# Kernel tuning notes

Measured on AMD Instinct MI355X. Metric: run time of the kernel, lower is better.

## Reference

```python
import jax, jax.numpy as jnp
import numpy as np

PI = float(np.pi)
TWO_PI = 2.0 * PI
LOG_2PI = float(np.log(TWO_PI))
N_FFT = 1024
LOG_N = 10
N_MAX = min(N_FFT, 2000)  # evaluate_z term cap


def _bitrev_indices(N, num_bits):
    idx = np.arange(N)
    rev = np.zeros(N, dtype=np.int32)
    v = idx.copy()
    for _ in range(num_bits):
        rev = (rev << 1) | (v & 1)
        v >>= 1
    return rev

_BITREV = jnp.asarray(_bitrev_indices(N_FFT, LOG_N))


def fft_fused(x_re, x_im):
    """Radix-2 DIT FFT with bit-reversal load, mirroring the Triton kernel.
    x_re/x_im: [B, N]. Returns (y_re, y_im)."""
    B, N = x_re.shape
    y = (x_re + 1j * x_im).astype(jnp.complex64)[:, _BITREV]
    for stage in range(LOG_N):
        s = 1 << stage          # half butterfly size (stride)
        # twiddles W_k = exp(-2*pi*i*k/(2s)), k in [0, s)
        k = jnp.arange(s)
        w = jnp.exp((-TWO_PI * 1j / (2 * s)) * k).astype(jnp.complex64)
        yg = y.reshape(B, N // (2 * s), 2, s)
        upper = yg[:, :, 0, :]
        lower = yg[:, :, 1, :] * w  # broadcast over [B, groups, s]
        y = jnp.concatenate([upper + lower, upper - lower], axis=-1).reshape(B, N)
    return jnp.real(y), jnp.imag(y)


def evaluate_z(t):
    """Riemann-Siegel Z(t) cosine sum with dynamic term count, masked."""
    t_half = t * 0.5
    theta = t_half * (jnp.log(t) - LOG_2PI) - t_half - PI / 8.0
    theta = theta + 1.0 / (48.0 * t)
    n = jnp.arange(1, N_MAX + 1, dtype=t.dtype)
    log_n = jnp.log(n)
    rsqrt_n = jax.lax.rsqrt(n)
    # [P, N_MAX] outer product of phases
    phases = t[:, None] * log_n[None, :] - theta[:, None]
    terms = rsqrt_n[None, :] * jnp.cos(phases)
    n_terms = jnp.clip(jnp.sqrt(jax.lax.stop_gradient(t) / TWO_PI).astype(jnp.int32), 10, N_MAX)
    mask = jnp.arange(N_MAX)[None, :] < n_terms[:, None]
    return 2.0 * jnp.sum(jnp.where(mask, terms, 0.0), axis=-1)


def setup_inputs() -> dict:
    key = jax.random.key(0)
    k1, k2, k3 = jax.random.split(key, 3)
    x_re = jax.random.normal(k1, (16384, N_FFT), dtype=jnp.float32)
    x_im = jax.random.normal(k2, (16384, N_FFT), dtype=jnp.float32)
    # evaluation points t in [1000, 101000)
    t = 1000.0 + 100000.0 * jax.random.uniform(k3, (262144,), dtype=jnp.float32)
    return {"x_re": x_re, "x_im": x_im, "t": t}


def reference(x_re, x_im, t):
    y_re, y_im = fft_fused(x_re, x_im)
    Z = evaluate_z(t)
    return (y_re, y_im, Z)
```

## Files before the change

### kernel.cpp

```cpp
#include <hip/hip_runtime.h>
#include <math.h>

#define INV_2PI_D 0.15915494309189535

#define LDSYNC() asm volatile("s_waitcnt lgkmcnt(0)" ::: "memory")

__device__ __forceinline__ void bfly(float& ar, float& ai, float& br, float& bi,
                                     float wr, float wi) {
    const float tr = wr * br - wi * bi;
    const float ti = wr * bi + wi * br;
    br = ar - tr; bi = ai - ti;
    ar = ar + tr; ai = ai + ti;
}

__device__ __forceinline__ void wrev(float rev, float& c, float& s) {
    s = __builtin_amdgcn_sinf(rev);
    c = __builtin_amdgcn_cosf(rev);
}

__device__ __forceinline__ void fft_row(
    const float* __restrict__ xre, const float* __restrict__ xim,
    float* __restrict__ yre, float* __restrict__ yim,
    float2* __restrict__ s,
    int row)
{
    const int lane = (int)(threadIdx.x & 63u);
    const size_t base = (size_t)row << 10;

    float re[16], im[16];

    const int rev6l = (int)(__brev((unsigned)lane) >> 26);
    const int REV4[16] = {0,8,4,12,2,10,6,14,1,9,5,13,3,11,7,15};
    const float* xr = xre + base + rev6l;
    const float* xi = xim + base + rev6l;
#pragma unroll
    for (int r = 0; r < 16; ++r) {
        re[r] = xr[REV4[r] << 6];
        im[r] = xi[REV4[r] << 6];
    }

    const int lo = lane & 15;
    const int hl = lane >> 4;
    const float lof = (float)lo;

    float c8a[8], s8a[8];
#pragma unroll
    for (int m = 0; m < 8; ++m)
        wrev(-(16.0f * (float)m + lof) * (1.0f / 256.0f), c8a[m], s8a[m]);
    float c4a[4], s4a[4];
#pragma unroll
    for (int m = 0; m < 4; ++m)
        wrev(-(16.0f * (float)m + lof) * (1.0f / 128.0f), c4a[m], s4a[m]);
    float c2a[2], s2a[2];
#pragma unroll
    for (int m = 0; m < 2; ++m)
        wrev(-(16.0f * (float)m + lof) * (1.0f / 64.0f), c2a[m], s2a[m]);
    float c1a, s1a;
    wrev(-lof * (1.0f / 32.0f), c1a, s1a);

    const float W8R[8] = {1.f, 0.9238795325112867f, 0.7071067811865476f,
                          0.3826834323650898f, 0.f, -0.3826834323650898f,
                          -0.7071067811865476f, -0.9238795325112867f};
    const float W8I[8] = {0.f, -0.3826834323650898f, -0.7071067811865476f,
                          -0.9238795325112867f, -1.f, -0.9238795325112867f,
                          -0.7071067811865476f, -0.3826834323650898f};
#pragma unroll
    for (int st = 0; st < 4; ++st) {
        const int S = 1 << st;
#pragma unroll
        for (int rl = 0; rl < 16; ++rl) {
            if (rl & S) continue;
            const int k8 = (rl & (S - 1)) * (8 >> st);
            bfly(re[rl], im[rl], re[rl | S], im[rl | S], W8R[k8], W8I[k8]);
        }
    }

    {
        float2* w = s + 17 * lane;
#pragma unroll
        for (int r = 0; r < 16; ++r) w[r] = make_float2(re[r], im[r]);
    }
    LDSYNC();
    float2* rw = s + 272 * hl + lo;
#pragma unroll
    for (int r = 0; r < 16; ++r) {
        const float2 v = rw[17 * r];
        re[r] = v.x; im[r] = v.y;
    }
    LDSYNC();

#pragma unroll
    for (int rl = 0; rl < 16; ++rl) if (!(rl & 1))
        bfly(re[rl], im[rl], re[rl|1], im[rl|1], c1a, s1a);
#pragma unroll
    for (int rl = 0; rl < 16; ++rl) if (!(rl & 2))
        bfly(re[rl], im[rl], re[rl|2], im[rl|2], c2a[rl & 1], s2a[rl & 1]);
#pragma unroll
    for (int rl = 0; rl < 16; ++rl) if (!(rl & 4))
        bfly(re[rl], im[rl], re[rl|4], im[rl|4], c4a[rl & 3], s4a[rl & 3]);
#pragma unroll
    for (int rl = 0; rl < 16; ++rl) if (!(rl & 8))
        bfly(re[rl], im[rl], re[rl|8], im[rl|8], c8a[rl & 7], s8a[rl & 7]);

    const float lf = (float)lane;
    float cz8[8], sz8[8];
#pragma unroll
    for (int m = 0; m < 8; ++m)
        wrev(-(64.0f * (float)m + lf) * (1.0f / 1024.0f), cz8[m], sz8[m]);
    float cz4[4], sz4[4];
#pragma unroll
    for (int m = 0; m < 4; ++m)
        wrev(-(64.0f * (float)m + lf) * (1.0f / 512.0f), cz4[m], sz4[m]);

#pragma unroll
    for (int r = 0; r < 16; ++r) rw[17 * r] = make_float2(re[r], im[r]);
    LDSYNC();
    {
        const float2* rb = s + 17 * hl + lo;
#pragma unroll
        for (int r = 0; r < 16; ++r) {
            const float2 v = rb[68 * r];
            re[r] = v.x; im[r] = v.y;
        }
    }
    LDSYNC();

#pragma unroll
    for (int rl = 0; rl < 16; ++rl) if (!(rl & 4))
        bfly(re[rl], im[rl], re[rl|4], im[rl|4], cz4[rl & 3], sz4[rl & 3]);
#pragma unroll
    for (int rl = 0; rl < 16; ++rl) if (!(rl & 8))
        bfly(re[rl], im[rl], re[rl|8], im[rl|8], cz8[rl & 7], sz8[rl & 7]);

    float* yr = yre + base + lane;
    float* yi = yim + base + lane;
#pragma unroll
    for (int r = 0; r < 16; ++r) {
        yr[r << 6] = re[r];
        yi[r << 6] = im[r];
    }
}

__global__ __launch_bounds__(256) void table_kernel(float* __restrict__ ws) {
    const int i = (int)(blockIdx.x * 256 + threadIdx.x);
    if (i < 1024) {
        const double nd = (double)(i + 1);
        ws[i]        = (float)log(nd);
        ws[1024 + i] = (float)(1.0 / sqrt(nd));
    }
}

__device__ void z_eval(const float* __restrict__ tin, float* __restrict__ zout,
                       const float* __restrict__ ws, int zblock, int n,
                       float* __restrict__ buf)
{
    for (int i = (int)threadIdx.x; i < 512; i += 256)
        reinterpret_cast<float4*>(buf)[i] = reinterpret_cast<const float4*>(ws)[i];
    __syncthreads();
    const float* slog = buf;
    const float* srsq = buf + 1024;

    const int gid = zblock * 256 + (int)threadIdx.x;
    if (gid >= n) return;

    const float t  = tin[gid];
    const float th = __fmul_rn(t, 0.5f);
    const float logt = (float)log((double)t);
    float theta = __fsub_rn(__fsub_rn(__fmul_rn(th, __fsub_rn(logt, 1.8378770664093453f)), th),
                            0.39269908169872414f);
    theta = __fadd_rn(theta, __fdiv_rn(1.0f, __fmul_rn(48.0f, t)));

    int nt = (int)sqrtf(__fdiv_rn(t, 6.283185307179586f));
    nt = min(max(nt, 10), 1024);

    float acc = 0.0f;
    for (int i = 0; i < nt; ++i) {
        const float p = __fsub_rn(__fmul_rn(t, slog[i]), theta);
        const double rev = (double)p * INV_2PI_D;
        const double fr  = rev - rint(rev);
        const float  c   = __builtin_amdgcn_cosf((float)fr);
        acc = __fmaf_rn(srsq[i], c, acc);
    }
    zout[gid] = __fmul_rn(2.0f, acc);
}

__global__ __launch_bounds__(256, 4) void fused_kernel(
    const float* __restrict__ xre, const float* __restrict__ xim,
    const float* __restrict__ tin, const float* __restrict__ ws,
    float* __restrict__ yre, float* __restrict__ yim, float* __restrict__ zout,
    int z_blocks, int nrows, int nz)
{
    __shared__ float2 s[4][1088];

    const int b = (int)blockIdx.x;
    if (b < z_blocks) {
        z_eval(tin, zout, ws, b, nz, reinterpret_cast<float*>(&s[0][0]));
    } else {
        const int wid = (int)(threadIdx.x >> 6);
        const int row = ((b - z_blocks) << 2) | wid;
        if (row < nrows)
            fft_row(xre, xim, yre, yim, s[wid], row);
    }
}

extern "C" void kernel_launch(void* const* d_in, const int* in_sizes, int n_in,
                              void* d_out, int out_size, void* d_ws, size_t ws_size,
                              hipStream_t stream)
{
    const float* xre = (const float*)d_in[0];
    const float* xim = (const float*)d_in[1];
    const float* t   = (const float*)d_in[2];

    const size_t nfft = (size_t)in_sizes[0];
    const int nrows = (int)(nfft >> 10);
    const int nz    = in_sizes[2];

    float* yre = (float*)d_out;
    float* yim = yre + nfft;
    float* z   = yre + 2 * nfft;
    float* ws  = (float*)d_ws;

    table_kernel<<<4, 256, 0, stream>>>(ws);

    const int f_blocks = (nrows + 3) >> 2;
    const int z_blocks = (nz + 255) >> 8;
    fused_kernel<<<z_blocks + f_blocks, 256, 0, stream>>>(
        xre, xim, t, ws, yre, yim, z, z_blocks, nrows, nz);
}
```

Baseline: 59.73 us.

## Replace LDS transposes in FFT with cross-lane DPP/swizzle butterfly stages

Restructures the per-row 1024-point FFT so the first six stages run across lanes using DPP moves, ds_swizzle and shfl_xor instead of two LDS transposes. Inputs are loaded as contiguous float4 vectors in a new bit-reversed mapping, and the last four stages stay in registers with per-stage twiddles. This removes the LDS traffic for the FFT and shrinks shared memory to the Z-table buffer only. In exchange each cross-lane stage computes both butterfly outputs per lane (roughly double the FLOPs) and adds many permute instructions.

```diff
diff --git a/kernel.cpp b/kernel.cpp
--- a/kernel.cpp
+++ b/kernel.cpp
@@ -3,7 +3,56 @@
 
 #define INV_2PI_D 0.15915494309189535
 
-#define LDSYNC() asm volatile("s_waitcnt lgkmcnt(0)" ::: "memory")
+__device__ __forceinline__ void wrev(float rev, float& c, float& s) {
+    s = __builtin_amdgcn_sinf(rev);
+    c = __builtin_amdgcn_cosf(rev);
+}
+
+template<int S>
+__device__ __forceinline__ float xshfl(float x) {
+    if constexpr (S == 1)
+        return __int_as_float(__builtin_amdgcn_mov_dpp(__float_as_int(x), 0xB1, 0xF, 0xF, true));
+    else if constexpr (S == 2)
+        return __int_as_float(__builtin_amdgcn_mov_dpp(__float_as_int(x), 0x4E, 0xF, 0xF, true));
+    else if constexpr (S == 8)
+        return __int_as_float(__builtin_amdgcn_mov_dpp(__float_as_int(x), 0x128, 0xF, 0xF, true));
+    else if constexpr (S == 4)
+        return __int_as_float(__builtin_amdgcn_ds_swizzle(__float_as_int(x), 0x101F));
+    else if constexpr (S == 16)
+        return __int_as_float(__builtin_amdgcn_ds_swizzle(__float_as_int(x), 0x401F));
+    else
+        return __shfl_xor(x, 32, 64);
+}
+
+template<int S>
+__device__ __forceinline__ void stage_x(float (&re)[16], float (&im)[16], int lane) {
+    float wr, wi;
+    wrev(-(float)(lane & (S - 1)) * (0.5f / (float)S), wr, wi);
+    const bool up = (lane & S) == 0;
+    const float c1r = up ? 1.0f : -wr;
+    const float c1i = up ? 0.0f : -wi;
+    const float c2r = up ? wr : 1.0f;
+    const float c2i = up ? wi : 0.0f;
+#pragma unroll
+    for (int r = 0; r < 16; ++r) {
+        const float pr = xshfl<S>(re[r]);
+        const float pi = xshfl<S>(im[r]);
+        const float a = re[r], b = im[r];
+        re[r] = a * c1r - b * c1i + pr * c2r - pi * c2i;
+        im[r] = a * c1i + b * c1r + pr * c2i + pi * c2r;
+    }
+}
+
+__device__ __forceinline__ void stage_x1(float (&re)[16], float (&im)[16], int lane) {
+    const float sgn = (lane & 1) ? -1.0f : 1.0f;
+#pragma unroll
+    for (int r = 0; r < 16; ++r) {
+        const float pr = xshfl<1>(re[r]);
+        const float pi = xshfl<1>(im[r]);
+        re[r] = __fmaf_rn(sgn, re[r], pr);
+        im[r] = __fmaf_rn(sgn, im[r], pi);
+    }
+}
 
 __device__ __forceinline__ void bfly(float& ar, float& ai, float& br, float& bi,
                                      float wr, float wi) {
@@ -13,16 +62,22 @@
     ar = ar + tr; ai = ai + ti;
 }
 
-__device__ __forceinline__ void wrev(float rev, float& c, float& s) {
-    s = __builtin_amdgcn_sinf(rev);
-    c = __builtin_amdgcn_cosf(rev);
+template<int M>
+__device__ __forceinline__ void stage_r(float (&re)[16], float (&im)[16], float lanef) {
+    float cw[M], sw[M];
+#pragma unroll
+    for (int m = 0; m < M; ++m)
+        wrev(-(64.0f * (float)m + lanef) * (1.0f / (128.0f * (float)M)), cw[m], sw[m]);
+#pragma unroll
+    for (int rl = 0; rl < 16; ++rl) {
+        if (rl & M) continue;
+        bfly(re[rl], im[rl], re[rl | M], im[rl | M], cw[rl & (M - 1)], sw[rl & (M - 1)]);
+    }
 }
 
 __device__ __forceinline__ void fft_row(
     const float* __restrict__ xre, const float* __restrict__ xim,
-    float* __restrict__ yre, float* __restrict__ yim,
-    float2* __restrict__ s,
-    int row)
+    float* __restrict__ yre, float* __restrict__ yim, int row)
 {
     const int lane = (int)(threadIdx.x & 63u);
     const size_t base = (size_t)row << 10;
@@ -30,107 +85,31 @@
     float re[16], im[16];
 
     const int rev6l = (int)(__brev((unsigned)lane) >> 26);
-    const int REV4[16] = {0,8,4,12,2,10,6,14,1,9,5,13,3,11,7,15};
-    const float* xr = xre + base + rev6l;
-    const float* xi = xim + base + rev6l;
-#pragma unroll
-    for (int r = 0; r < 16; ++r) {
-        re[r] = xr[REV4[r] << 6];
-        im[r] = xi[REV4[r] << 6];
-    }
-
-    const int lo = lane & 15;
-    const int hl = lane >> 4;
-    const float lof = (float)lo;
-
-    float c8a[8], s8a[8];
-#pragma unroll
-    for (int m = 0; m < 8; ++m)
-        wrev(-(16.0f * (float)m + lof) * (1.0f / 256.0f), c8a[m], s8a[m]);
-    float c4a[4], s4a[4];
-#pragma unroll
-    for (int m = 0; m < 4; ++m)
-        wrev(-(16.0f * (float)m + lof) * (1.0f / 128.0f), c4a[m], s4a[m]);
-    float c2a[2], s2a[2];
-#pragma unroll
-    for (int m = 0; m < 2; ++m)
-        wrev(-(16.0f * (float)m + lof) * (1.0f / 64.0f), c2a[m], s2a[m]);
-    float c1a, s1a;
-    wrev(-lof * (1.0f / 32.0f), c1a, s1a);
-
-    const float W8R[8] = {1.f, 0.9238795325112867f, 0.7071067811865476f,
-                          0.3826834323650898f, 0.f, -0.3826834323650898f,
-                          -0.7071067811865476f, -0.9238795325112867f};
-    const float W8I[8] = {0.f, -0.3826834323650898f, -0.7071067811865476f,
-                          -0.9238795325112867f, -1.f, -0.9238795325112867f,
-                          -0.7071067811865476f, -0.3826834323650898f};
-#pragma unroll
-    for (int st = 0; st < 4; ++st) {
-        const int S = 1 << st;
-#pragma unroll
-        for (int rl = 0; rl < 16; ++rl) {
-            if (rl & S) continue;
-            const int k8 = (rl & (S - 1)) * (8 >> st);
-            bfly(re[rl], im[rl], re[rl | S], im[rl | S], W8R[k8], W8I[k8]);
-        }
-    }
-
-    {
-        float2* w = s + 17 * lane;
-#pragma unroll
-        for (int r = 0; r < 16; ++r) w[r] = make_float2(re[r], im[r]);
-    }
-    LDSYNC();
-    float2* rw = s + 272 * hl + lo;
-#pragma unroll
-    for (int r = 0; r < 16; ++r) {
-        const float2 v = rw[17 * r];
-        re[r] = v.x; im[r] = v.y;
-    }
-    LDSYNC();
-
-#pragma unroll
-    for (int rl = 0; rl < 16; ++rl) if (!(rl & 1))
-        bfly(re[rl], im[rl], re[rl|1], im[rl|1], c1a, s1a);
-#pragma unroll
-    for (int rl = 0; rl < 16; ++rl) if (!(rl & 2))
-        bfly(re[rl], im[rl], re[rl|2], im[rl|2], c2a[rl & 1], s2a[rl & 1]);
-#pragma unroll
-    for (int rl = 0; rl < 16; ++rl) if (!(rl & 4))
-        bfly(re[rl], im[rl], re[rl|4], im[rl|4], c4a[rl & 3], s4a[rl & 3]);
-#pragma unroll
-    for (int rl = 0; rl < 16; ++rl) if (!(rl & 8))
-        bfly(re[rl], im[rl], re[rl|8], im[rl|8], c8a[rl & 7], s8a[rl & 7]);
-
-    const float lf = (float)lane;
-    float cz8[8], sz8[8];
-#pragma unroll
-    for (int m = 0; m < 8; ++m)
-        wrev(-(64.0f * (float)m + lf) * (1.0f / 1024.0f), cz8[m], sz8[m]);
-    float cz4[4], sz4[4];
-#pragma unroll
-    for (int m = 0; m < 4; ++m)
-        wrev(-(64.0f * (float)m + lf) * (1.0f / 512.0f), cz4[m], sz4[m]);
-
-#pragma unroll
-    for (int r = 0; r < 16; ++r) rw[17 * r] = make_float2(re[r], im[r]);
-    LDSYNC();
-    {
-        const float2* rb = s + 17 * hl + lo;
-#pragma unroll
-        for (int r = 0; r < 16; ++r) {
-            const float2 v = rb[68 * r];
-            re[r] = v.x; im[r] = v.y;
-        }
-    }
-    LDSYNC();
-
-#pragma unroll
-    for (int rl = 0; rl < 16; ++rl) if (!(rl & 4))
-        bfly(re[rl], im[rl], re[rl|4], im[rl|4], cz4[rl & 3], sz4[rl & 3]);
-#pragma unroll
-    for (int rl = 0; rl < 16; ++rl) if (!(rl & 8))
-        bfly(re[rl], im[rl], re[rl|8], im[rl|8], cz8[rl & 7], sz8[rl & 7]);
+    const float4* xr4 = reinterpret_cast<const float4*>(xre + base) + (rev6l << 2);
+    const float4* xi4 = reinterpret_cast<const float4*>(xim + base) + (rev6l << 2);
+
+    static constexpr int RM[4][4] = {
+        {0, 8, 4, 12}, {2, 10, 6, 14}, {1, 9, 5, 13}, {3, 11, 7, 15}};
+#pragma unroll
+    for (int q = 0; q < 4; ++q) {
+        const float4 vr = xr4[q];
+        const float4 vi = xi4[q];
+        re[RM[q][0]] = vr.x; re[RM[q][1]] = vr.y; re[RM[q][2]] = vr.z; re[RM[q][3]] = vr.w;
+        im[RM[q][0]] = vi.x; im[RM[q][1]] = vi.y; im[RM[q][2]] = vi.z; im[RM[q][3]] = vi.w;
+    }
+
+    stage_x1(re, im, lane);
+    stage_x<2>(re, im, lane);
+    stage_x<4>(re, im, lane);
+    stage_x<8>(re, im, lane);
+    stage_x<16>(re, im, lane);
+    stage_x<32>(re, im, lane);
+
+    const float lanef = (float)lane;
+    stage_r<1>(re, im, lanef);
+    stage_r<2>(re, im, lanef);
+    stage_r<4>(re, im, lanef);
+    stage_r<8>(re, im, lanef);
 
     float* yr = yre + base + lane;
     float* yi = yim + base + lane;
@@ -190,16 +169,16 @@
     float* __restrict__ yre, float* __restrict__ yim, float* __restrict__ zout,
     int z_blocks, int nrows, int nz)
 {
-    __shared__ float2 s[4][1088];
+    __shared__ float zbuf[2048];
 
     const int b = (int)blockIdx.x;
     if (b < z_blocks) {
-        z_eval(tin, zout, ws, b, nz, reinterpret_cast<float*>(&s[0][0]));
+        z_eval(tin, zout, ws, b, nz, zbuf);
     } else {
         const int wid = (int)(threadIdx.x >> 6);
         const int row = ((b - z_blocks) << 2) | wid;
         if (row < nrows)
-            fft_row(xre, xim, yre, yim, s[wid], row);
+            fft_row(xre, xim, yre, yim, row);
     }
 }
 
```

After: 58.64 us. About the same (-1.8%).
